# Optimization experiments

Hardware: AMD Instinct MI355X
Metric: run time of the kernel (lower is better)

## Reference

```python
import jax, jax.numpy as jnp
import numpy as np

H = 32  # hidden_size
I = 1   # input_size
O = 1   # output_size


def setup_inputs() -> dict:
    key = jax.random.key(0)
    ks = jax.random.split(key, 7)
    T, B = 2048, 2048
    s_ih = 1.0 / np.sqrt(H)
    return {
        "x": jax.random.normal(ks[0], (T, B, I), dtype=jnp.float32),
        "W_ih": jax.random.uniform(ks[1], (4 * H, I), jnp.float32, -s_ih, s_ih),
        "W_hh": jax.random.uniform(ks[2], (4 * H, H), jnp.float32, -s_ih, s_ih),
        "b_ih": jax.random.uniform(ks[3], (4 * H,), jnp.float32, -s_ih, s_ih),
        "b_hh": jax.random.uniform(ks[4], (4 * H,), jnp.float32, -s_ih, s_ih),
        "W_out": jax.random.uniform(ks[5], (O, H), jnp.float32, -s_ih, s_ih),
        "b_out": jax.random.uniform(ks[6], (O,), jnp.float32, -s_ih, s_ih),
    }


def _lstm(x, W_ih, W_hh, b_ih, b_hh):
    T, B, _ = x.shape
    # Precompute input contribution for all timesteps: [T, B, 4H]
    x_gates = jnp.einsum('tbi,gi->tbg', x, W_ih) + b_ih + b_hh

    def step(carry, xg):
        h, c = carry
        gates = xg + h @ W_hh.T  # [B, 4H]
        i, f, g, o = jnp.split(gates, 4, axis=-1)  # PyTorch gate order i,f,g,o
        i = jax.nn.sigmoid(i)
        f = jax.nn.sigmoid(f)
        g = jnp.tanh(g)
        o = jax.nn.sigmoid(o)
        c = f * c + i * g
        h = o * jnp.tanh(c)
        return (h, c), h

    h0 = jnp.zeros((B, H), dtype=x.dtype)
    c0 = jnp.zeros((B, H), dtype=x.dtype)
    (hT, cT), r_out = jax.lax.scan(step, (h0, c0), x_gates)
    return r_out, (hT[None], cT[None])  # match PyTorch [num_layers, B, H] state


def reference(x, W_ih, W_hh, b_ih, b_hh, W_out, b_out):
    r_out, state = _lstm(x, W_ih, W_hh, b_ih, b_hh)  # [T, B, H]
    outs = jnp.einsum('tbh,oh->tbo', r_out, W_out) + b_out  # [T, B, O]
    return outs, state
```

## Files before the change

### kernel.cpp

```cpp
#include <hip/hip_runtime.h>


namespace {
constexpr int T_ = 2048;
constexpr int B_ = 2048;
constexpr int H_ = 32;
constexpr int WPB = 4;
constexpr int EPB = WPB * 2;
constexpr int CHUNK = 32;
constexpr int NCH = T_ / CHUNK;
constexpr int OUTS = T_ * B_;
constexpr float L2E = 1.442695040888963f;

typedef float v2f __attribute__((ext_vector_type(2)));
typedef float v4f __attribute__((ext_vector_type(4)));

__device__ __forceinline__ float rcp_(float v){ return __builtin_amdgcn_rcpf(v); }
__device__ __forceinline__ float ex2_(float v){ return __builtin_amdgcn_exp2f(v); }

template <int CTRL, int RM, int BM, bool BC>
__device__ __forceinline__ float dpp_add(float acc, float src) {
    int mv = __builtin_amdgcn_update_dpp(0, __builtin_bit_cast(int, src),
                                         CTRL, RM, BM, BC);
    return acc + __builtin_bit_cast(float, mv);
}
__device__ __forceinline__ float half_sum32(float v) {
    v = dpp_add<0x111, 0xF, 0xF, true >(v, v);
    v = dpp_add<0x112, 0xF, 0xF, true >(v, v);
    v = dpp_add<0x114, 0xF, 0xF, true >(v, v);
    v = dpp_add<0x118, 0xF, 0xF, true >(v, v);
    v = dpp_add<0x142, 0xA, 0xF, false>(v, v);
    return v;
}
}

__global__ __launch_bounds__(256, 1)
__attribute__((amdgpu_waves_per_eu(1, 1)))
void lstm_fused7(
    const float* __restrict__ x,
    const float* __restrict__ W_ih,
    const float* __restrict__ W_hh,
    const float* __restrict__ b_ih,
    const float* __restrict__ b_hh,
    const float* __restrict__ W_out,
    const float* __restrict__ b_out,
    float* __restrict__ out)
{
    const int l  = threadIdx.x & 63;
    const int wv = threadIdx.x >> 6;
    const int j  = l & 31;
    const int p  = l >> 5;
    const int e  = blockIdx.x * EPB + wv * 2 + p;

    __shared__ __align__(16) float hbuf[WPB][2][H_];

    const float sI = -L2E, sF = -L2E, sG = 2.0f * L2E, sO = -L2E;

    v2f wi[H_/2], wf[H_/2], wg[H_/2], wo[H_/2];
#pragma unroll
    for (int k2 = 0; k2 < H_/2; ++k2) {
        const float* ri = W_hh + (0*H_ + j) * H_;
        const float* rf = W_hh + (1*H_ + j) * H_;
        const float* rg = W_hh + (2*H_ + j) * H_;
        const float* ro = W_hh + (3*H_ + j) * H_;
        wi[k2] = (v2f){ ri[2*k2] * sI, ri[2*k2+1] * sI };
        wf[k2] = (v2f){ rf[2*k2] * sF, rf[2*k2+1] * sF };
        wg[k2] = (v2f){ rg[2*k2] * sG, rg[2*k2+1] * sG };
        wo[k2] = (v2f){ ro[2*k2] * sO, ro[2*k2+1] * sO };
    }

    const float wxi = W_ih[0*H_+j] * sI, wxf = W_ih[1*H_+j] * sF;
    const float wxg = W_ih[2*H_+j] * sG, wxo = W_ih[3*H_+j] * sO;
    const float bi  = (b_ih[0*H_+j] + b_hh[0*H_+j]) * sI;
    const float bf  = (b_ih[1*H_+j] + b_hh[1*H_+j]) * sF;
    const float bg  = (b_ih[2*H_+j] + b_hh[2*H_+j]) * sG;
    const float bo_ = (b_ih[3*H_+j] + b_hh[3*H_+j]) * sO;
    const float wout = W_out[j];
    const float bout = b_out[0];

    float c = 0.0f, h = 0.0f;
    hbuf[wv][p][j] = 0.0f;
    __asm__ __volatile__("" ::: "memory");
    v4f hq[H_/4];
#pragma unroll
    for (int q = 0; q < H_/4; ++q)
        hq[q] = ((const v4f*)&hbuf[wv][p][0])[q];

    float xcur = x[j * B_ + e];
    int outOff = e;

    for (int ch = 0; ch < NCH; ++ch) {
        float xnext = 0.0f;
        if (ch + 1 < NCH) xnext = x[((ch + 1) * CHUNK + j) * B_ + e];
#pragma unroll 8
        for (int s = 0; s < CHUNK; ++s) {
#pragma unroll
            for (int k2 = 0; k2 < H_/2; ++k2) {
                __asm__ __volatile__("" : "+v"(wi[k2]));
                __asm__ __volatile__("" : "+v"(wf[k2]));
                __asm__ __volatile__("" : "+v"(wg[k2]));
                __asm__ __volatile__("" : "+v"(wo[k2]));
            }
            const int xr0 = __builtin_amdgcn_readlane(__builtin_bit_cast(int, xcur), s);
            const int xr1 = __builtin_amdgcn_readlane(__builtin_bit_cast(int, xcur), s + 32);
            const float xk = p ? __builtin_bit_cast(float, xr1)
                               : __builtin_bit_cast(float, xr0);
            v2f ai0 = {bi  + xk * wxi, 0.f}, ai1 = {0.f, 0.f};
            v2f af0 = {bf  + xk * wxf, 0.f}, af1 = {0.f, 0.f};
            v2f ag0 = {bg  + xk * wxg, 0.f}, ag1 = {0.f, 0.f};
            v2f ao0 = {bo_ + xk * wxo, 0.f}, ao1 = {0.f, 0.f};
#pragma unroll
            for (int q = 0; q < H_/4; ++q) {
                const v2f hlo = (v2f){ hq[q].x, hq[q].y };
                const v2f hhi = (v2f){ hq[q].z, hq[q].w };
                ai0 += wi[2*q] * hlo;  ai1 += wi[2*q+1] * hhi;
                af0 += wf[2*q] * hlo;  af1 += wf[2*q+1] * hhi;
                ag0 += wg[2*q] * hlo;  ag1 += wg[2*q+1] * hhi;
                ao0 += wo[2*q] * hlo;  ao1 += wo[2*q+1] * hhi;
            }
            const v2f ai = ai0 + ai1, af = af0 + af1;
            const v2f ag = ag0 + ag1, ao = ao0 + ao1;
            const float iv = rcp_(1.0f + ex2_(ai.x + ai.y));
            const float fv = rcp_(1.0f + ex2_(af.x + af.y));
            const float gv = 1.0f - 2.0f * rcp_(1.0f + ex2_(ag.x + ag.y));
            const float ov = rcp_(1.0f + ex2_(ao.x + ao.y));
            c = fv * c + iv * gv;
            const float tc = 1.0f - 2.0f * rcp_(1.0f + ex2_((2.0f * L2E) * c));
            h = ov * tc;
            hbuf[wv][p][j] = h;
            __asm__ __volatile__("" ::: "memory");
#pragma unroll
            for (int q = 0; q < H_/4; ++q)
                hq[q] = ((const v4f*)&hbuf[wv][p][0])[q];
            const float pr = half_sum32(h * wout);
            if ((l & 31) == 31) out[outOff] = pr + bout;
            outOff += B_;
        }
        xcur = xnext;
    }
    out[OUTS + e * H_ + j] = h;
    out[OUTS + B_ * H_ + e * H_ + j] = c;
}

extern "C" void kernel_launch(void* const* d_in, const int* in_sizes, int n_in,
                              void* d_out, int out_size, void* d_ws, size_t ws_size,
                              hipStream_t stream) {
    const float* x     = (const float*)d_in[0];
    const float* W_ih  = (const float*)d_in[1];
    const float* W_hh  = (const float*)d_in[2];
    const float* b_ih  = (const float*)d_in[3];
    const float* b_hh  = (const float*)d_in[4];
    const float* W_out = (const float*)d_in[5];
    const float* b_out = (const float*)d_in[6];
    lstm_fused7<<<dim3(B_ / EPB), dim3(256), 0, stream>>>(
        x, W_ih, W_hh, b_ih, b_hh, W_out, b_out, (float*)d_out);
}
```

Before: 723.6 us.

## Broadcast hidden state via DPP row rotates and ds_swizzle instead of LDS

Replaces the per-step LDS write/read of the hidden vector with register-level exchange: 16 DPP row-rotate moves within each 16-lane row plus a ds_swizzle to fetch the other half, with W_hh weights pre-permuted per lane to match the rotated order. This removes LDS round-trip latency on the serial recurrence path. In exchange, packed v2f FMAs become scalar FMAs (more instructions), each DPP move adds latency and ds_swizzle still uses the LDS crossbar. Unroll is reduced from 8 to 4.

After: 792.5 us. +9.5%, slower.

```diff
diff --git a/kernel.cpp b/kernel.cpp
--- a/kernel.cpp
+++ b/kernel.cpp
@@ -12,31 +12,32 @@
 constexpr int OUTS = T_ * B_;
 constexpr float L2E = 1.442695040888963f;
 
-typedef float v2f __attribute__((ext_vector_type(2)));
-typedef float v4f __attribute__((ext_vector_type(4)));
-
 __device__ __forceinline__ float rcp_(float v){ return __builtin_amdgcn_rcpf(v); }
 __device__ __forceinline__ float ex2_(float v){ return __builtin_amdgcn_exp2f(v); }
 
 template <int CTRL, int RM, int BM, bool BC>
+__device__ __forceinline__ float dpp_movf(float src) {
+    return __builtin_bit_cast(float,
+        __builtin_amdgcn_update_dpp(0, __builtin_bit_cast(int, src),
+                                    CTRL, RM, BM, BC));
+}
+template <int CTRL, int RM, int BM, bool BC>
 __device__ __forceinline__ float dpp_add(float acc, float src) {
-    int mv = __builtin_amdgcn_update_dpp(0, __builtin_bit_cast(int, src),
-                                         CTRL, RM, BM, BC);
-    return acc + __builtin_bit_cast(float, mv);
+    return acc + dpp_movf<CTRL,RM,BM,BC>(src);
 }
 __device__ __forceinline__ float half_sum32(float v) {
-    v = dpp_add<0x111, 0xF, 0xF, true >(v, v);
-    v = dpp_add<0x112, 0xF, 0xF, true >(v, v);
-    v = dpp_add<0x114, 0xF, 0xF, true >(v, v);
-    v = dpp_add<0x118, 0xF, 0xF, true >(v, v);
-    v = dpp_add<0x142, 0xA, 0xF, false>(v, v);
+    v = dpp_add<0x111,0xF,0xF,true >(v, v);
+    v = dpp_add<0x112,0xF,0xF,true >(v, v);
+    v = dpp_add<0x114,0xF,0xF,true >(v, v);
+    v = dpp_add<0x118,0xF,0xF,true >(v, v);
+    v = dpp_add<0x142,0xA,0xF,false>(v, v);
     return v;
 }
 }
 
 __global__ __launch_bounds__(256, 1)
 __attribute__((amdgpu_waves_per_eu(1, 1)))
-void lstm_fused7(
+void lstm_fused9(
     const float* __restrict__ x,
     const float* __restrict__ W_ih,
     const float* __restrict__ W_hh,
@@ -51,95 +52,99 @@
     const int j  = l & 31;
     const int p  = l >> 5;
     const int e  = blockIdx.x * EPB + wv * 2 + p;
+    const int jl = l & 15;
+    const int rowoff   = j & 16;
+    const int otheroff = 16 - rowoff;
 
-    __shared__ __align__(16) float hbuf[WPB][2][H_];
+    const float sI = -L2E, sF = -L2E, sG = 2.0f*L2E, sO = -L2E;
 
-    const float sI = -L2E, sF = -L2E, sG = 2.0f * L2E, sO = -L2E;
-
-    v2f wi[H_/2], wf[H_/2], wg[H_/2], wo[H_/2];
+    float wI[32], wF[32], wG[32], wO[32];
 #pragma unroll
-    for (int k2 = 0; k2 < H_/2; ++k2) {
-        const float* ri = W_hh + (0*H_ + j) * H_;
-        const float* rf = W_hh + (1*H_ + j) * H_;
-        const float* rg = W_hh + (2*H_ + j) * H_;
-        const float* ro = W_hh + (3*H_ + j) * H_;
-        wi[k2] = (v2f){ ri[2*k2] * sI, ri[2*k2+1] * sI };
-        wf[k2] = (v2f){ rf[2*k2] * sF, rf[2*k2+1] * sF };
-        wg[k2] = (v2f){ rg[2*k2] * sG, rg[2*k2+1] * sG };
-        wo[k2] = (v2f){ ro[2*k2] * sO, ro[2*k2+1] * sO };
+    for (int r = 0; r < 16; ++r) {
+        const int ks = rowoff   + ((jl - r) & 15);
+        const int kx = otheroff + ((jl - r) & 15);
+        wI[r]    = W_hh[(0*H_+j)*H_ + ks] * sI;
+        wI[16+r] = W_hh[(0*H_+j)*H_ + kx] * sI;
+        wF[r]    = W_hh[(1*H_+j)*H_ + ks] * sF;
+        wF[16+r] = W_hh[(1*H_+j)*H_ + kx] * sF;
+        wG[r]    = W_hh[(2*H_+j)*H_ + ks] * sG;
+        wG[16+r] = W_hh[(2*H_+j)*H_ + kx] * sG;
+        wO[r]    = W_hh[(3*H_+j)*H_ + ks] * sO;
+        wO[16+r] = W_hh[(3*H_+j)*H_ + kx] * sO;
+    }
+#pragma unroll
+    for (int r = 0; r < 32; ++r) {
+        __asm__ __volatile__("" : "+v"(wI[r]), "+v"(wF[r]));
+        __asm__ __volatile__("" : "+v"(wG[r]), "+v"(wO[r]));
     }
 
-    const float wxi = W_ih[0*H_+j] * sI, wxf = W_ih[1*H_+j] * sF;
-    const float wxg = W_ih[2*H_+j] * sG, wxo = W_ih[3*H_+j] * sO;
-    const float bi  = (b_ih[0*H_+j] + b_hh[0*H_+j]) * sI;
-    const float bf  = (b_ih[1*H_+j] + b_hh[1*H_+j]) * sF;
-    const float bg  = (b_ih[2*H_+j] + b_hh[2*H_+j]) * sG;
-    const float bo_ = (b_ih[3*H_+j] + b_hh[3*H_+j]) * sO;
+    const float wxI = W_ih[0*H_+j]*sI, wxF = W_ih[1*H_+j]*sF;
+    const float wxG = W_ih[2*H_+j]*sG, wxO = W_ih[3*H_+j]*sO;
+    const float bI = (b_ih[0*H_+j]+b_hh[0*H_+j])*sI;
+    const float bF = (b_ih[1*H_+j]+b_hh[1*H_+j])*sF;
+    const float bG = (b_ih[2*H_+j]+b_hh[2*H_+j])*sG;
+    const float bO = (b_ih[3*H_+j]+b_hh[3*H_+j])*sO;
     const float wout = W_out[j];
     const float bout = b_out[0];
 
     float c = 0.0f, h = 0.0f;
-    hbuf[wv][p][j] = 0.0f;
-    __asm__ __volatile__("" ::: "memory");
-    v4f hq[H_/4];
-#pragma unroll
-    for (int q = 0; q < H_/4; ++q)
-        hq[q] = ((const v4f*)&hbuf[wv][p][0])[q];
-
     float xcur = x[j * B_ + e];
     int outOff = e;
 
     for (int ch = 0; ch < NCH; ++ch) {
         float xnext = 0.0f;
-        if (ch + 1 < NCH) xnext = x[((ch + 1) * CHUNK + j) * B_ + e];
-#pragma unroll 8
+        if (ch + 1 < NCH) xnext = x[((ch+1)*CHUNK + j) * B_ + e];
+#pragma unroll 4
         for (int s = 0; s < CHUNK; ++s) {
-#pragma unroll
-            for (int k2 = 0; k2 < H_/2; ++k2) {
-                __asm__ __volatile__("" : "+v"(wi[k2]));
-                __asm__ __volatile__("" : "+v"(wf[k2]));
-                __asm__ __volatile__("" : "+v"(wg[k2]));
-                __asm__ __volatile__("" : "+v"(wo[k2]));
-            }
+            const float hs = __builtin_bit_cast(float,
+                __builtin_amdgcn_ds_swizzle(__builtin_bit_cast(int, h), 0x401F));
             const int xr0 = __builtin_amdgcn_readlane(__builtin_bit_cast(int, xcur), s);
             const int xr1 = __builtin_amdgcn_readlane(__builtin_bit_cast(int, xcur), s + 32);
             const float xk = p ? __builtin_bit_cast(float, xr1)
                                : __builtin_bit_cast(float, xr0);
-            v2f ai0 = {bi  + xk * wxi, 0.f}, ai1 = {0.f, 0.f};
-            v2f af0 = {bf  + xk * wxf, 0.f}, af1 = {0.f, 0.f};
-            v2f ag0 = {bg  + xk * wxg, 0.f}, ag1 = {0.f, 0.f};
-            v2f ao0 = {bo_ + xk * wxo, 0.f}, ao1 = {0.f, 0.f};
-#pragma unroll
-            for (int q = 0; q < H_/4; ++q) {
-                const v2f hlo = (v2f){ hq[q].x, hq[q].y };
-                const v2f hhi = (v2f){ hq[q].z, hq[q].w };
-                ai0 += wi[2*q] * hlo;  ai1 += wi[2*q+1] * hhi;
-                af0 += wf[2*q] * hlo;  af1 += wf[2*q+1] * hhi;
-                ag0 += wg[2*q] * hlo;  ag1 += wg[2*q+1] * hhi;
-                ao0 += wo[2*q] * hlo;  ao1 += wo[2*q+1] * hhi;
-            }
-            const v2f ai = ai0 + ai1, af = af0 + af1;
-            const v2f ag = ag0 + ag1, ao = ao0 + ao1;
-            const float iv = rcp_(1.0f + ex2_(ai.x + ai.y));
-            const float fv = rcp_(1.0f + ex2_(af.x + af.y));
-            const float gv = 1.0f - 2.0f * rcp_(1.0f + ex2_(ag.x + ag.y));
-            const float ov = rcp_(1.0f + ex2_(ao.x + ao.y));
-            c = fv * c + iv * gv;
-            const float tc = 1.0f - 2.0f * rcp_(1.0f + ex2_((2.0f * L2E) * c));
-            h = ov * tc;
-            hbuf[wv][p][j] = h;
-            __asm__ __volatile__("" ::: "memory");
-#pragma unroll
-            for (int q = 0; q < H_/4; ++q)
-                hq[q] = ((const v4f*)&hbuf[wv][p][0])[q];
+            float aI0 = bI + xk*wxI, aI1 = 0.f, aI2 = 0.f, aI3 = 0.f;
+            float aF0 = bF + xk*wxF, aF1 = 0.f, aF2 = 0.f, aF3 = 0.f;
+            float aG0 = bG + xk*wxG, aG1 = 0.f, aG2 = 0.f, aG3 = 0.f;
+            float aO0 = bO + xk*wxO, aO1 = 0.f, aO2 = 0.f, aO3 = 0.f;
+            aI0 += wI[0]*h; aF0 += wF[0]*h; aG0 += wG[0]*h; aO0 += wO[0]*h;
+#define ROR_STEP(R, IDX)                                                     \
+            { const float hr_ = dpp_movf<0x120+(R),0xF,0xF,true>(h);         \
+              aI##IDX += wI[R]*hr_; aF##IDX += wF[R]*hr_;                    \
+              aG##IDX += wG[R]*hr_; aO##IDX += wO[R]*hr_; }
+            ROR_STEP(1,1)  ROR_STEP(2,2)  ROR_STEP(3,3)
+            ROR_STEP(4,0)  ROR_STEP(5,1)  ROR_STEP(6,2)  ROR_STEP(7,3)
+            ROR_STEP(8,0)  ROR_STEP(9,1)  ROR_STEP(10,2) ROR_STEP(11,3)
+            ROR_STEP(12,0) ROR_STEP(13,1) ROR_STEP(14,2) ROR_STEP(15,3)
+#undef ROR_STEP
+            aI0 += wI[16]*hs; aF0 += wF[16]*hs; aG0 += wG[16]*hs; aO0 += wO[16]*hs;
+#define RORX_STEP(R, IDX)                                                    \
+            { const float hr_ = dpp_movf<0x120+(R),0xF,0xF,true>(hs);        \
+              aI##IDX += wI[16+(R)]*hr_; aF##IDX += wF[16+(R)]*hr_;          \
+              aG##IDX += wG[16+(R)]*hr_; aO##IDX += wO[16+(R)]*hr_; }
+            RORX_STEP(1,1)  RORX_STEP(2,2)  RORX_STEP(3,3)
+            RORX_STEP(4,0)  RORX_STEP(5,1)  RORX_STEP(6,2)  RORX_STEP(7,3)
+            RORX_STEP(8,0)  RORX_STEP(9,1)  RORX_STEP(10,2) RORX_STEP(11,3)
+            RORX_STEP(12,0) RORX_STEP(13,1) RORX_STEP(14,2) RORX_STEP(15,3)
+#undef RORX_STEP
+            const float aI = (aI0+aI1)+(aI2+aI3);
+            const float aF = (aF0+aF1)+(aF2+aF3);
+            const float aG = (aG0+aG1)+(aG2+aG3);
+            const float aO = (aO0+aO1)+(aO2+aO3);
+            const float iv = rcp_(1.0f + ex2_(aI));
+            const float fv = rcp_(1.0f + ex2_(aF));
+            const float gv = 1.0f - 2.0f*rcp_(1.0f + ex2_(aG));
+            const float ov = rcp_(1.0f + ex2_(aO));
+            c = fv*c + iv*gv;
+            const float tc = 1.0f - 2.0f*rcp_(1.0f + ex2_((2.0f*L2E)*c));
+            h = ov*tc;
             const float pr = half_sum32(h * wout);
             if ((l & 31) == 31) out[outOff] = pr + bout;
             outOff += B_;
         }
         xcur = xnext;
     }
-    out[OUTS + e * H_ + j] = h;
-    out[OUTS + B_ * H_ + e * H_ + j] = c;
+    out[OUTS + e*H_ + j] = h;
+    out[OUTS + B_*H_ + e*H_ + j] = c;
 }
 
 extern "C" void kernel_launch(void* const* d_in, const int* in_sizes, int n_in,
@@ -152,6 +157,6 @@
     const float* b_hh  = (const float*)d_in[4];
     const float* W_out = (const float*)d_in[5];
     const float* b_out = (const float*)d_in[6];
-    lstm_fused7<<<dim3(B_ / EPB), dim3(256), 0, stream>>>(
+    lstm_fused9<<<dim3(B_ / EPB), dim3(256), 0, stream>>>(
         x, W_ih, W_hh, b_ih, b_hh, W_out, b_out, (float*)d_out);
 }
```
